# Kernel tuning notes

Measured on AMD Instinct MI355X. Metric: run time of the kernel, lower is better.

Reference implementation:

```python
import jax, jax.numpy as jnp
import numpy as np

E, C, D = 8, 8192, 1024
B, S = 8, 4096

def setup_inputs() -> dict:
    key = jax.random.key(0)
    k1, k2, k3 = jax.random.split(key, 3)
    expert_outputs = jax.random.normal(k1, (E, C, D), dtype=jnp.float32)
    weights = jax.random.uniform(k2, (E, C), dtype=jnp.float32)
    token_indices = jax.random.randint(k3, (E, C), 0, B * S, dtype=jnp.int64)
    return {
        "expert_outputs": expert_outputs,
        "weights": weights,
        "token_indices": token_indices,
        "batch_size": B,
        "seq_len": S,
    }

def reference(expert_outputs, weights, token_indices, batch_size, seq_len):
    # expert_outputs: [E, C, D], weights: [E, C], token_indices: [E, C] in [0, B*S)
    n_tokens = batch_size * seq_len
    out_dim = expert_outputs.shape[-1]
    # weight each expert's outputs, then scatter-add into the flat token buffer
    weighted = expert_outputs * weights[..., None]              # [E, C, D]
    flat = jnp.zeros((n_tokens, out_dim), dtype=expert_outputs.dtype)
    flat = flat.at[token_indices.reshape(-1)].add(weighted.reshape(-1, out_dim))
    return flat.reshape(batch_size, seq_len, out_dim)
```

## Files before the change

### kernel.cpp

```cpp
#include <hip/hip_runtime.h>

#define E_EXP 8
#define C_CAP 8192
#define D_DIM 1024
#define N_ROWS (E_EXP * C_CAP)
#define N_TOK  (8 * 4096)
#define SLOTS_K 16
#define WPB 4
#define GATHER_BLOCKS (N_TOK / WPB)

typedef float f32x4 __attribute__((ext_vector_type(4)));

__device__ __forceinline__ f32x4 ld4(const float* p) {
    return *reinterpret_cast<const f32x4*>(p);
}

__global__ __launch_bounds__(256) void combine_build(
    const int* __restrict__ token_indices,
    int* __restrict__ count,
    unsigned short* __restrict__ slots)
{
    const int row = blockIdx.x * 256 + threadIdx.x;
    const int tok = token_indices[row];
    const int slot = atomicAdd(&count[tok], 1);
    if (slot < SLOTS_K) {
        slots[(size_t)tok * SLOTS_K + slot] = (unsigned short)row;
    }
}

template<int N>
__device__ __forceinline__ void gather_rows(const float* __restrict__ eo,
                                            const float* __restrict__ w,
                                            const unsigned short* __restrict__ id,
                                            int lane, f32x4 acc[4])
{
    int row[N];
    #pragma unroll
    for (int r = 0; r < N; ++r) row[r] = id[r];
    float wt[N];
    #pragma unroll
    for (int r = 0; r < N; ++r) wt[r] = w[row[r]];
    f32x4 v[N][4];
    #pragma unroll
    for (int r = 0; r < N; ++r) {
        const float* base = eo + (size_t)row[r] * D_DIM + lane * 4;
        #pragma unroll
        for (int c = 0; c < 4; ++c)
            v[r][c] = ld4(base + c * 256);
    }
    #pragma unroll
    for (int r = 0; r < N; ++r) {
        #pragma unroll
        for (int c = 0; c < 4; ++c) acc[c] += wt[r] * v[r][c];
    }
}

__global__ __launch_bounds__(256) void combine_gather(
    const float* __restrict__ expert_outputs,
    const float* __restrict__ weights,
    const int* __restrict__ token_indices,
    const int* __restrict__ count,
    const unsigned short* __restrict__ slots,
    float* __restrict__ out)
{
    const int wv   = threadIdx.x >> 6;
    const int lane = threadIdx.x & 63;
    const int tok  = blockIdx.x * WPB + wv;

    const int n = count[tok];
    const unsigned short* sl = slots + (size_t)tok * SLOTS_K;

    f32x4 acc[4];
    #pragma unroll
    for (int c = 0; c < 4; ++c) acc[c] = (f32x4)(0.f);

    if (__builtin_expect(n <= SLOTS_K, 1)) {
        switch (n) {
        case 0: break;
        case 1: gather_rows<1>(expert_outputs, weights, sl, lane, acc); break;
        case 2: gather_rows<2>(expert_outputs, weights, sl, lane, acc); break;
        case 3: gather_rows<3>(expert_outputs, weights, sl, lane, acc); break;
        default: {
            int r = 0;
            for (; r + 2 <= n; r += 2)
                gather_rows<2>(expert_outputs, weights, sl + r, lane, acc);
            if (r < n)
                gather_rows<1>(expert_outputs, weights, sl + r, lane, acc);
        } }
    } else {
        for (int row = 0; row < N_ROWS; ++row) {
            if (token_indices[row] == tok) {
                const float w = weights[row];
                const float* base = expert_outputs + (size_t)row * D_DIM + lane * 4;
                #pragma unroll
                for (int c = 0; c < 4; ++c) acc[c] += w * ld4(base + c * 256);
            }
        }
    }

    float* ob = out + (size_t)tok * D_DIM + lane * 4;
    #pragma unroll
    for (int c = 0; c < 4; ++c)
        __builtin_nontemporal_store(acc[c], reinterpret_cast<f32x4*>(ob + c * 256));
}

extern "C" void kernel_launch(void* const* d_in, const int* in_sizes, int n_in,
                              void* d_out, int out_size, void* d_ws, size_t ws_size,
                              hipStream_t stream) {
    const float* expert_outputs = (const float*)d_in[0];
    const float* weights        = (const float*)d_in[1];
    const int*   token_indices  = (const int*)d_in[2];
    float* out = (float*)d_out;

    int* count = (int*)d_ws;
    unsigned short* slots = (unsigned short*)(count + N_TOK);

    hipMemsetAsync(count, 0, (size_t)N_TOK * sizeof(int), stream);

    combine_build<<<N_ROWS / 256, 256, 0, stream>>>(
        token_indices, count, slots);

    combine_gather<<<GATHER_BLOCKS, 256, 0, stream>>>(
        expert_outputs, weights, token_indices, count, slots, out);
}
```

Before: 74.44 us.

## Fuse slot-build and gather into one persistent kernel with grid barrier

Merges the bucket-building kernel and the gather kernel into a single launch of 1024 blocks. Blocks first insert rows into per-token slot lists, then meet at a software grid barrier (atomic counter plus spin), and each wave then processes 8 tokens in a loop. This removes one kernel launch and the inter-kernel gap, at the cost of spin-wait overhead and a dependence on all 1024 blocks being co-resident, since the barrier deadlocks otherwise. It also cuts the gather grid from 8192 blocks to 1024.

Result: slower. 156.9 us (+110.8%).

```diff
diff --git a/kernel.cpp b/kernel.cpp
--- a/kernel.cpp
+++ b/kernel.cpp
@@ -6,26 +6,14 @@
 #define N_ROWS (E_EXP * C_CAP)
 #define N_TOK  (8 * 4096)
 #define SLOTS_K 16
-#define WPB 4
-#define GATHER_BLOCKS (N_TOK / WPB)
+#define NBLK 1024
+#define TOK_PER_BLK (N_TOK / NBLK)
+#define TOK_PER_WAVE (TOK_PER_BLK / 4)
 
 typedef float f32x4 __attribute__((ext_vector_type(4)));
 
 __device__ __forceinline__ f32x4 ld4(const float* p) {
     return *reinterpret_cast<const f32x4*>(p);
-}
-
-__global__ __launch_bounds__(256) void combine_build(
-    const int* __restrict__ token_indices,
-    int* __restrict__ count,
-    unsigned short* __restrict__ slots)
-{
-    const int row = blockIdx.x * 256 + threadIdx.x;
-    const int tok = token_indices[row];
-    const int slot = atomicAdd(&count[tok], 1);
-    if (slot < SLOTS_K) {
-        slots[(size_t)tok * SLOTS_K + slot] = (unsigned short)row;
-    }
 }
 
 template<int N>
@@ -55,53 +43,78 @@
     }
 }
 
-__global__ __launch_bounds__(256) void combine_gather(
+__global__ __launch_bounds__(256, 4) void combine_fused(
     const float* __restrict__ expert_outputs,
     const float* __restrict__ weights,
     const int* __restrict__ token_indices,
-    const int* __restrict__ count,
-    const unsigned short* __restrict__ slots,
+    int* __restrict__ count,
+    unsigned short* __restrict__ slots,
+    int* __restrict__ bar,
     float* __restrict__ out)
 {
+    const int tid = blockIdx.x * 256 + threadIdx.x;
+
+    if (tid < N_ROWS) {
+        const int tok = token_indices[tid];
+        const int slot = atomicAdd(&count[tok], 1);
+        if (slot < SLOTS_K)
+            slots[(size_t)tok * SLOTS_K + slot] = (unsigned short)tid;
+    }
+
+    __syncthreads();
+    if (threadIdx.x == 0) {
+        __hip_atomic_fetch_add(bar, 1, __ATOMIC_RELEASE,
+                               __HIP_MEMORY_SCOPE_AGENT);
+        while (__hip_atomic_load(bar, __ATOMIC_ACQUIRE,
+                                 __HIP_MEMORY_SCOPE_AGENT) < NBLK)
+            __builtin_amdgcn_s_sleep(2);
+    }
+    __syncthreads();
+
     const int wv   = threadIdx.x >> 6;
     const int lane = threadIdx.x & 63;
-    const int tok  = blockIdx.x * WPB + wv;
+    const int tokBase = blockIdx.x * TOK_PER_BLK + wv * TOK_PER_WAVE;
 
-    const int n = count[tok];
-    const unsigned short* sl = slots + (size_t)tok * SLOTS_K;
+    for (int j = 0; j < TOK_PER_WAVE; ++j) {
+        const int tok = tokBase + j;
+        const int n = count[tok];
+        const unsigned short* sl = slots + (size_t)tok * SLOTS_K;
 
-    f32x4 acc[4];
-    #pragma unroll
-    for (int c = 0; c < 4; ++c) acc[c] = (f32x4)(0.f);
+        f32x4 acc[4];
+        #pragma unroll
+        for (int c = 0; c < 4; ++c) acc[c] = (f32x4)(0.f);
 
-    if (__builtin_expect(n <= SLOTS_K, 1)) {
-        switch (n) {
-        case 0: break;
-        case 1: gather_rows<1>(expert_outputs, weights, sl, lane, acc); break;
-        case 2: gather_rows<2>(expert_outputs, weights, sl, lane, acc); break;
-        case 3: gather_rows<3>(expert_outputs, weights, sl, lane, acc); break;
-        default: {
-            int r = 0;
-            for (; r + 2 <= n; r += 2)
-                gather_rows<2>(expert_outputs, weights, sl + r, lane, acc);
-            if (r < n)
-                gather_rows<1>(expert_outputs, weights, sl + r, lane, acc);
-        } }
-    } else {
-        for (int row = 0; row < N_ROWS; ++row) {
-            if (token_indices[row] == tok) {
-                const float w = weights[row];
-                const float* base = expert_outputs + (size_t)row * D_DIM + lane * 4;
-                #pragma unroll
-                for (int c = 0; c < 4; ++c) acc[c] += w * ld4(base + c * 256);
+        if (__builtin_expect(n <= SLOTS_K, 1)) {
+            switch (n) {
+            case 0: break;
+            case 1: gather_rows<1>(expert_outputs, weights, sl, lane, acc); break;
+            case 2: gather_rows<2>(expert_outputs, weights, sl, lane, acc); break;
+            case 3: gather_rows<3>(expert_outputs, weights, sl, lane, acc); break;
+            default: {
+                int r = 0;
+                for (; r + 2 <= n; r += 2)
+                    gather_rows<2>(expert_outputs, weights, sl + r, lane, acc);
+                if (r < n)
+                    gather_rows<1>(expert_outputs, weights, sl + r, lane, acc);
+            } }
+        } else {
+            for (int row = 0; row < N_ROWS; ++row) {
+                if (token_indices[row] == tok) {
+                    const float w = weights[row];
+                    const float* base =
+                        expert_outputs + (size_t)row * D_DIM + lane * 4;
+                    #pragma unroll
+                    for (int c = 0; c < 4; ++c) acc[c] += w * ld4(base + c * 256);
+                }
             }
         }
+
+        float* ob = out + (size_t)tok * D_DIM + lane * 4;
+        #pragma unroll
+        for (int c = 0; c < 4; ++c)
+            __builtin_nontemporal_store(acc[c],
+                reinterpret_cast<f32x4*>(ob + c * 256));
     }
-
-    float* ob = out + (size_t)tok * D_DIM + lane * 4;
-    #pragma unroll
-    for (int c = 0; c < 4; ++c)
-        __builtin_nontemporal_store(acc[c], reinterpret_cast<f32x4*>(ob + c * 256));
 }
 
 extern "C" void kernel_launch(void* const* d_in, const int* in_sizes, int n_in,
@@ -113,13 +126,11 @@
     float* out = (float*)d_out;
 
     int* count = (int*)d_ws;
-    unsigned short* slots = (unsigned short*)(count + N_TOK);
+    int* bar   = count + N_TOK;
+    unsigned short* slots = (unsigned short*)(bar + 1);
 
-    hipMemsetAsync(count, 0, (size_t)N_TOK * sizeof(int), stream);
+    hipMemsetAsync(count, 0, (size_t)(N_TOK + 1) * sizeof(int), stream);
 
-    combine_build<<<N_ROWS / 256, 256, 0, stream>>>(
-        token_indices, count, slots);
-
-    combine_gather<<<GATHER_BLOCKS, 256, 0, stream>>>(
-        expert_outputs, weights, token_indices, count, slots, out);
+    combine_fused<<<NBLK, 256, 0, stream>>>(
+        expert_outputs, weights, token_indices, count, slots, bar, out);
 }
```

## Process four tokens per wave with prefetched slot lists and register-held indices

Applied to the files above, without the earlier changes.

Each wavefront now handles four consecutive tokens instead of one, cutting the grid by four. The 16 slot indices for a token are loaded as two uint4 vectors and unpacked in registers, and the next token's slots and count are prefetched while the current token is gathered. Row counts up to 16 dispatch to fully unrolled templates. This aims to hide the index-load latency ahead of the gathers, at the cost of fewer waves in flight and higher register pressure.

Result: no change. 74.30 us, median of 2 (-0.2%).

```diff
diff --git a/kernel.cpp b/kernel.cpp
--- a/kernel.cpp
+++ b/kernel.cpp
@@ -6,8 +6,8 @@
 #define N_ROWS (E_EXP * C_CAP)
 #define N_TOK  (8 * 4096)
 #define SLOTS_K 16
-#define WPB 4
-#define GATHER_BLOCKS (N_TOK / WPB)
+#define WV_TOK 4
+#define GATHER_BLOCKS (N_TOK / (4 * WV_TOK))
 
 typedef float f32x4 __attribute__((ext_vector_type(4)));
 
@@ -28,31 +28,55 @@
     }
 }
 
+__device__ __forceinline__ unsigned pickw(const uint4& a, const uint4& b, int w) {
+    unsigned r = a.x;
+    r = (w == 1) ? a.y : r; r = (w == 2) ? a.z : r; r = (w == 3) ? a.w : r;
+    r = (w == 4) ? b.x : r; r = (w == 5) ? b.y : r; r = (w == 6) ? b.z : r;
+    r = (w == 7) ? b.w : r;
+    return r;
+}
+__device__ __forceinline__ int sid(const uint4& a, const uint4& b, int r) {
+    const unsigned word = pickw(a, b, r >> 1);
+    return (r & 1) ? (int)(word >> 16) : (int)(word & 0xFFFFu);
+}
+
 template<int N>
 __device__ __forceinline__ void gather_rows(const float* __restrict__ eo,
-                                            const float* __restrict__ w,
-                                            const unsigned short* __restrict__ id,
-                                            int lane, f32x4 acc[4])
+                                            const float* __restrict__ wts,
+                                            const uint4& sa, const uint4& sb,
+                                            int base, int lane, f32x4 acc[4])
 {
     int row[N];
     #pragma unroll
-    for (int r = 0; r < N; ++r) row[r] = id[r];
+    for (int r = 0; r < N; ++r) row[r] = sid(sa, sb, base + r);
     float wt[N];
     #pragma unroll
-    for (int r = 0; r < N; ++r) wt[r] = w[row[r]];
+    for (int r = 0; r < N; ++r) wt[r] = wts[row[r]];
     f32x4 v[N][4];
     #pragma unroll
     for (int r = 0; r < N; ++r) {
-        const float* base = eo + (size_t)row[r] * D_DIM + lane * 4;
+        const float* bp = eo + (size_t)row[r] * D_DIM + lane * 4;
         #pragma unroll
-        for (int c = 0; c < 4; ++c)
-            v[r][c] = ld4(base + c * 256);
+        for (int c = 0; c < 4; ++c) v[r][c] = ld4(bp + c * 256);
     }
     #pragma unroll
     for (int r = 0; r < N; ++r) {
         #pragma unroll
         for (int c = 0; c < 4; ++c) acc[c] += wt[r] * v[r][c];
     }
+}
+
+template<int NN>
+__device__ __forceinline__ void gather_n(const float* __restrict__ eo,
+                                         const float* __restrict__ wts,
+                                         const uint4& sa, const uint4& sb,
+                                         int lane, f32x4 acc[4])
+{
+    #pragma unroll
+    for (int r = 0; r + 2 <= NN; r += 2)
+        gather_rows<2>(eo, wts, sa, sb, r, lane, acc);
+    if constexpr (NN & 1)
+        gather_rows<1>(eo, wts, sa, sb, NN - 1, lane, acc);
 }
 
 __global__ __launch_bounds__(256) void combine_gather(
@@ -65,43 +89,67 @@
 {
     const int wv   = threadIdx.x >> 6;
     const int lane = threadIdx.x & 63;
-    const int tok  = blockIdx.x * WPB + wv;
+    int tok = blockIdx.x * (4 * WV_TOK) + wv * WV_TOK;
 
-    const int n = count[tok];
-    const unsigned short* sl = slots + (size_t)tok * SLOTS_K;
+    const uint4* sp = reinterpret_cast<const uint4*>(slots);
 
-    f32x4 acc[4];
+    uint4 sa = sp[2 * tok], sb = sp[2 * tok + 1];
+    int ncur = count[tok];
+
     #pragma unroll
-    for (int c = 0; c < 4; ++c) acc[c] = (f32x4)(0.f);
+    for (int j = 0; j < WV_TOK; ++j) {
+        uint4 na = {0, 0, 0, 0}, nb = {0, 0, 0, 0};
+        int nn = 0;
+        if (j < WV_TOK - 1) {
+            na = sp[2 * (tok + 1)];
+            nb = sp[2 * (tok + 1) + 1];
+            nn = count[tok + 1];
+        }
 
-    if (__builtin_expect(n <= SLOTS_K, 1)) {
-        switch (n) {
-        case 0: break;
-        case 1: gather_rows<1>(expert_outputs, weights, sl, lane, acc); break;
-        case 2: gather_rows<2>(expert_outputs, weights, sl, lane, acc); break;
-        case 3: gather_rows<3>(expert_outputs, weights, sl, lane, acc); break;
-        default: {
-            int r = 0;
-            for (; r + 2 <= n; r += 2)
-                gather_rows<2>(expert_outputs, weights, sl + r, lane, acc);
-            if (r < n)
-                gather_rows<1>(expert_outputs, weights, sl + r, lane, acc);
-        } }
-    } else {
-        for (int row = 0; row < N_ROWS; ++row) {
-            if (token_indices[row] == tok) {
-                const float w = weights[row];
-                const float* base = expert_outputs + (size_t)row * D_DIM + lane * 4;
-                #pragma unroll
-                for (int c = 0; c < 4; ++c) acc[c] += w * ld4(base + c * 256);
+        f32x4 acc[4];
+        #pragma unroll
+        for (int c = 0; c < 4; ++c) acc[c] = (f32x4)(0.f);
+
+        if (__builtin_expect(ncur <= SLOTS_K, 1)) {
+            switch (ncur) {
+            case 0: break;
+            case 1:  gather_n<1>(expert_outputs, weights, sa, sb, lane, acc); break;
+            case 2:  gather_n<2>(expert_outputs, weights, sa, sb, lane, acc); break;
+            case 3:  gather_n<3>(expert_outputs, weights, sa, sb, lane, acc); break;
+            case 4:  gather_n<4>(expert_outputs, weights, sa, sb, lane, acc); break;
+            case 5:  gather_n<5>(expert_outputs, weights, sa, sb, lane, acc); break;
+            case 6:  gather_n<6>(expert_outputs, weights, sa, sb, lane, acc); break;
+            case 7:  gather_n<7>(expert_outputs, weights, sa, sb, lane, acc); break;
+            case 8:  gather_n<8>(expert_outputs, weights, sa, sb, lane, acc); break;
+            case 9:  gather_n<9>(expert_outputs, weights, sa, sb, lane, acc); break;
+            case 10: gather_n<10>(expert_outputs, weights, sa, sb, lane, acc); break;
+            case 11: gather_n<11>(expert_outputs, weights, sa, sb, lane, acc); break;
+            case 12: gather_n<12>(expert_outputs, weights, sa, sb, lane, acc); break;
+            case 13: gather_n<13>(expert_outputs, weights, sa, sb, lane, acc); break;
+            case 14: gather_n<14>(expert_outputs, weights, sa, sb, lane, acc); break;
+            case 15: gather_n<15>(expert_outputs, weights, sa, sb, lane, acc); break;
+            default: gather_n<16>(expert_outputs, weights, sa, sb, lane, acc); break;
+            }
+        } else {
+            for (int row = 0; row < N_ROWS; ++row) {
+                if (token_indices[row] == tok) {
+                    const float w = weights[row];
+                    const float* bp =
+                        expert_outputs + (size_t)row * D_DIM + lane * 4;
+                    #pragma unroll
+                    for (int c = 0; c < 4; ++c) acc[c] += w * ld4(bp + c * 256);
+                }
             }
         }
+
+        float* ob = out + (size_t)tok * D_DIM + lane * 4;
+        #pragma unroll
+        for (int c = 0; c < 4; ++c)
+            __builtin_nontemporal_store(acc[c],
+                reinterpret_cast<f32x4*>(ob + c * 256));
+
+        sa = na; sb = nb; ncur = nn; ++tok;
     }
-
-    float* ob = out + (size_t)tok * D_DIM + lane * 4;
-    #pragma unroll
-    for (int c = 0; c < 4; ++c)
-        __builtin_nontemporal_store(acc[c], reinterpret_cast<f32x4*>(ob + c * 256));
 }
 
 extern "C" void kernel_launch(void* const* d_in, const int* in_sizes, int n_in,
```
